# Kernel tuning notes

Hardware: AMD Instinct MI355X
Metric: run time of the kernel (lower is better)

The kernel has to match this reference:

```python
import jax, jax.numpy as jnp
import numpy as np

N_NODES = 50000
N_EDGES = 800000
D_IN = 96
D_HID = 256
D_OUT = 2
N_GRAPHS = 64


def _gin_conv(x, src, dst, W1, b1, W2, b2):
    # GINConv with eps=0: MLP(x + sum_{j in N(i)} x_j)
    agg = jax.ops.segment_sum(x[src], dst, num_segments=x.shape[0])
    h = x + agg
    h = jax.nn.relu(h @ W1 + b1)
    return h @ W2 + b2


def setup_inputs() -> dict:
    key = jax.random.key(0)
    ks = jax.random.split(key, 12)
    x = jax.random.normal(ks[0], (N_NODES, D_IN), dtype=jnp.float32)
    edge_index = jax.random.randint(ks[1], (2, N_EDGES), 0, N_NODES, dtype=jnp.int64)
    batch = jnp.sort(jax.random.randint(ks[2], (N_NODES,), 0, N_GRAPHS, dtype=jnp.int64))

    def lin(k, fan_in, shape):
        bound = 1.0 / np.sqrt(fan_in)
        return jax.random.uniform(k, shape, jnp.float32, -bound, bound)

    W1 = lin(ks[3], D_IN, (D_IN, D_HID)); b1 = lin(ks[4], D_IN, (D_HID,))
    W2 = lin(ks[5], D_HID, (D_HID, D_HID)); b2 = lin(ks[6], D_HID, (D_HID,))
    V1 = lin(ks[7], D_HID, (D_HID, D_HID)); c1 = lin(ks[8], D_HID, (D_HID,))
    V2 = lin(ks[9], D_HID, (D_HID, D_HID)); c2 = lin(ks[10], D_HID, (D_HID,))
    Wl = lin(ks[11], D_HID, (D_HID, D_OUT)); bl = jnp.zeros((D_OUT,), jnp.float32)
    return {"x": x, "edge_index": edge_index, "batch": batch,
            "W1": W1, "b1": b1, "W2": W2, "b2": b2,
            "V1": V1, "c1": c1, "V2": V2, "c2": c2,
            "Wl": Wl, "bl": bl}


def reference(x, edge_index, batch, W1, b1, W2, b2, V1, c1, V2, c2, Wl, bl):
    src, dst = edge_index[0], edge_index[1]
    h = jax.nn.relu(_gin_conv(x, src, dst, W1, b1, W2, b2))
    h = _gin_conv(h, src, dst, V1, c1, V2, c2)
    # global_mean_pool over batch ids
    sums = jax.ops.segment_sum(h, batch, num_segments=N_GRAPHS)
    counts = jax.ops.segment_sum(jnp.ones((h.shape[0], 1), h.dtype), batch,
                                 num_segments=N_GRAPHS)
    pooled = sums / jnp.maximum(counts, 1.0)
    # dropout p=0.1 is identity in eval mode
    return pooled @ Wl + bl
```

## Files before the change

### kernel.cpp

```cpp
#include <hip/hip_runtime.h>

#define N_NODES 50000
#define N_EDGES 800000
#define D_IN 96
#define D_HID 256
#define N_GRAPHS 64

#define SCAN_NB ((N_NODES + 255) / 256)

typedef __attribute__((ext_vector_type(8))) short bf16x8;
typedef __attribute__((ext_vector_type(4))) float f32x4;

__device__ __forceinline__ unsigned short f2bf(float f) {
    union { float f; unsigned int u; } v; v.f = f;
    unsigned int r = (v.u + 0x7FFFu + ((v.u >> 16) & 1u)) >> 16;
    return (unsigned short)r;
}
__device__ __forceinline__ float bfLo(unsigned int u) {
    union { unsigned int u; float f; } v; v.u = u << 16; return v.f;
}
__device__ __forceinline__ float bfHi(unsigned int u) {
    union { unsigned int u; float f; } v; v.u = u & 0xFFFF0000u; return v.f;
}
__device__ __forceinline__ unsigned int packbf(float a, float b) {
    return (unsigned int)f2bf(a) | ((unsigned int)f2bf(b) << 16);
}

__global__ void k_count(const int* __restrict__ dst, int* __restrict__ deg, int E) {
    int e = blockIdx.x * blockDim.x + threadIdx.x;
    if (e < E) atomicAdd(&deg[dst[e]], 1);
}

__global__ __launch_bounds__(256) void k_scan1(const int* __restrict__ deg,
                                               int* __restrict__ bsum, int n) {
    __shared__ int red[256];
    int tid = threadIdx.x;
    int i = blockIdx.x * 256 + tid;
    red[tid] = (i < n) ? deg[i] : 0;
    __syncthreads();
    for (int off = 128; off > 0; off >>= 1) {
        if (tid < off) red[tid] += red[tid + off];
        __syncthreads();
    }
    if (tid == 0) bsum[blockIdx.x] = red[0];
}

__global__ __launch_bounds__(256) void k_scan2(int* __restrict__ bsum, int nb) {
    __shared__ int s[256];
    int tid = threadIdx.x;
    int v = (tid < nb) ? bsum[tid] : 0;
    s[tid] = v;
    __syncthreads();
    for (int off = 1; off < 256; off <<= 1) {
        int t = (tid >= off) ? s[tid - off] : 0;
        __syncthreads();
        s[tid] += t;
        __syncthreads();
    }
    if (tid < nb) bsum[tid] = s[tid] - v;
}

__global__ __launch_bounds__(256) void k_scan3(const int* __restrict__ deg,
                                               const int* __restrict__ bsum,
                                               int* __restrict__ rp,
                                               int* __restrict__ wp, int n) {
    __shared__ int s[256];
    int tid = threadIdx.x;
    int i = blockIdx.x * 256 + tid;
    int v = (i < n) ? deg[i] : 0;
    s[tid] = v;
    __syncthreads();
    for (int off = 1; off < 256; off <<= 1) {
        int t = (tid >= off) ? s[tid - off] : 0;
        __syncthreads();
        s[tid] += t;
        __syncthreads();
    }
    if (i < n) {
        int excl = s[tid] - v + bsum[blockIdx.x];
        rp[i] = excl;
        wp[i] = excl;
    }
    if (blockIdx.x == 0 && tid == 0) rp[n] = N_EDGES;
}

__global__ void k_scatter(const int* __restrict__ src, const int* __restrict__ dst,
                          int* __restrict__ wp, int* __restrict__ csr, int E) {
    int e = blockIdx.x * blockDim.x + threadIdx.x;
    if (e < E) {
        int p = atomicAdd(&wp[dst[e]], 1);
        csr[p] = src[e];
    }
}

__global__ __launch_bounds__(256) void k_x2bf(const float* __restrict__ x,
                                              unsigned short* __restrict__ xb, int n4) {
    int i = blockIdx.x * 256 + threadIdx.x;
    if (i >= n4) return;
    float4 v = ((const float4*)x)[i];
    ((uint2*)xb)[i] = make_uint2(packbf(v.x, v.y), packbf(v.z, v.w));
}

#define ACCUM(acc, v)                                    \
    do {                                                 \
        acc[0] += bfLo((v).x); acc[1] += bfHi((v).x);    \
        acc[2] += bfLo((v).y); acc[3] += bfHi((v).y);    \
        acc[4] += bfLo((v).z); acc[5] += bfHi((v).z);    \
        acc[6] += bfLo((v).w); acc[7] += bfHi((v).w);    \
    } while (0)

__global__ __launch_bounds__(256) void k_agg96b(const unsigned short* __restrict__ xb,
                                                const int* __restrict__ rp,
                                                const int* __restrict__ csr,
                                                unsigned short* __restrict__ h0, int n) {
    int wid = blockIdx.x * 4 + (threadIdx.x >> 6);
    if (wid >= n) return;
    int lane = threadIdx.x & 63;
    int grp = lane / 12;
    int sub = lane % 12;
    int s = rp[wid], e = rp[wid + 1];
    const uint4* xp = (const uint4*)xb;
    float a[8] = {0.f, 0.f, 0.f, 0.f, 0.f, 0.f, 0.f, 0.f};
    float b[8] = {0.f, 0.f, 0.f, 0.f, 0.f, 0.f, 0.f, 0.f};
    if (lane < 48) {
        int j = s + grp;
        for (; j + 4 < e; j += 8) {
            int sc0 = csr[j];
            int sc1 = csr[j + 4];
            uint4 v0 = xp[(size_t)sc0 * 12 + sub];
            uint4 v1 = xp[(size_t)sc1 * 12 + sub];
            ACCUM(a, v0);
            ACCUM(b, v1);
        }
        if (j < e) {
            int sc0 = csr[j];
            uint4 v0 = xp[(size_t)sc0 * 12 + sub];
            ACCUM(a, v0);
        }
    }
#pragma unroll
    for (int i = 0; i < 8; i++) a[i] += b[i];
#pragma unroll
    for (int i = 0; i < 8; i++) a[i] += __shfl(a[i], lane + 24, 64);
#pragma unroll
    for (int i = 0; i < 8; i++) a[i] += __shfl(a[i], lane + 12, 64);
    if (lane < 12) {
        uint4 v = xp[(size_t)wid * 12 + sub];
        ACCUM(a, v);
        uint4 o;
        o.x = packbf(a[0], a[1]); o.y = packbf(a[2], a[3]);
        o.z = packbf(a[4], a[5]); o.w = packbf(a[6], a[7]);
        ((uint4*)h0)[(size_t)wid * 12 + sub] = o;
    }
}

__global__ __launch_bounds__(256) void k_agg256b(const unsigned short* __restrict__ h,
                                                 const int* __restrict__ rp,
                                                 const int* __restrict__ csr,
                                                 unsigned short* __restrict__ outb, int n) {
    int wid = blockIdx.x * 4 + (threadIdx.x >> 6);
    if (wid >= n) return;
    int lane = threadIdx.x & 63;
    int half = lane >> 5;
    int sub = lane & 31;
    int s = rp[wid], e = rp[wid + 1];
    const uint4* hp = (const uint4*)h;
    float a[8] = {0.f, 0.f, 0.f, 0.f, 0.f, 0.f, 0.f, 0.f};
    float b[8] = {0.f, 0.f, 0.f, 0.f, 0.f, 0.f, 0.f, 0.f};
    int j = s + half;
    for (; j + 2 < e; j += 4) {
        int sc0 = csr[j];
        int sc1 = csr[j + 2];
        uint4 v0 = hp[(size_t)sc0 * 32 + sub];
        uint4 v1 = hp[(size_t)sc1 * 32 + sub];
        ACCUM(a, v0);
        ACCUM(b, v1);
    }
    if (j < e) {
        int sc0 = csr[j];
        uint4 v0 = hp[(size_t)sc0 * 32 + sub];
        ACCUM(a, v0);
    }
#pragma unroll
    for (int i = 0; i < 8; i++) a[i] += b[i];
#pragma unroll
    for (int i = 0; i < 8; i++) a[i] += __shfl(a[i], sub + 32, 64);
    if (half == 0) {
        uint4 v = hp[(size_t)wid * 32 + sub];
        ACCUM(a, v);
        uint4 o;
        o.x = packbf(a[0], a[1]); o.y = packbf(a[2], a[3]);
        o.z = packbf(a[4], a[5]); o.w = packbf(a[6], a[7]);
        ((uint4*)outb)[(size_t)wid * 32 + sub] = o;
    }
}

__global__ __launch_bounds__(256) void k_wt(const float* __restrict__ W,
                                            unsigned short* __restrict__ Wt, int K) {
    int idx = blockIdx.x * 256 + threadIdx.x;
    if (idx >= K * 256) return;
    int k = idx >> 8;
    int n = idx & 255;
    Wt[(size_t)n * K + k] = f2bf(W[idx]);
}

template <int K1, bool RELU2>
__global__ __launch_bounds__(256) void fused_mlp(const unsigned short* __restrict__ A,
                                                 const unsigned short* __restrict__ W1t,
                                                 const float* __restrict__ bias1,
                                                 const unsigned short* __restrict__ W2t,
                                                 const float* __restrict__ bias2,
                                                 unsigned short* __restrict__ C, int M) {
    __shared__ unsigned short As[64][72];
    __shared__ unsigned short Bs[256][72];
    __shared__ unsigned short T1[64][264];
    const int tid = threadIdx.x;
    const int lane = tid & 63;
    const int wid = tid >> 6;
    const int wm = wid >> 1;
    const int wn = wid & 1;
    const int row0 = blockIdx.x * 64;

    f32x4 acc[2][8];
#pragma unroll
    for (int f = 0; f < 2; f++)
#pragma unroll
        for (int g = 0; g < 8; g++) acc[f][g] = (f32x4){0.f, 0.f, 0.f, 0.f};

    for (int kt = 0; kt < K1; kt += 64) {
        __syncthreads();
        {
            int m = tid >> 2;
            int kc = (tid & 3) * 16;
            int gr = row0 + m;
            uint4 w0 = make_uint4(0u, 0u, 0u, 0u), w1 = w0;
            int k = kt + kc;
            if (gr < M && k < K1) {
                w0 = *(const uint4*)&A[(size_t)gr * K1 + k];
                if (k + 8 < K1) w1 = *(const uint4*)&A[(size_t)gr * K1 + k + 8];
            }
            uint4* dst = (uint4*)&As[m][kc];
            dst[0] = w0; dst[1] = w1;
        }
#pragma unroll
        for (int p = 0; p < 2; p++) {
            int n = (tid >> 1) + p * 128;
            int kc = (tid & 1) * 32;
            uint4 w[4];
#pragma unroll
            for (int i = 0; i < 4; i++) {
                int k = kt + kc + i * 8;
                w[i] = (k < K1) ? *(const uint4*)&W1t[(size_t)n * K1 + k]
                                : make_uint4(0u, 0u, 0u, 0u);
            }
            uint4* dst = (uint4*)&Bs[n][kc];
#pragma unroll
            for (int i = 0; i < 4; i++) dst[i] = w[i];
        }
        __syncthreads();
#pragma unroll
        for (int ks = 0; ks < 2; ks++) {
            int ko = ks * 32 + (lane >> 4) * 8;
            bf16x8 af[2], bfr[8];
#pragma unroll
            for (int f = 0; f < 2; f++)
                af[f] = *(const bf16x8*)&As[wm * 32 + f * 16 + (lane & 15)][ko];
#pragma unroll
            for (int g = 0; g < 8; g++)
                bfr[g] = *(const bf16x8*)&Bs[wn * 128 + g * 16 + (lane & 15)][ko];
#pragma unroll
            for (int f = 0; f < 2; f++)
#pragma unroll
                for (int g = 0; g < 8; g++)
                    acc[f][g] = __builtin_amdgcn_mfma_f32_16x16x32_bf16(
                        af[f], bfr[g], acc[f][g], 0, 0, 0);
        }
    }

#pragma unroll
    for (int g = 0; g < 8; g++) {
        int col = wn * 128 + g * 16 + (lane & 15);
        float bb = bias1[col];
#pragma unroll
        for (int f = 0; f < 2; f++) {
#pragma unroll
            for (int r = 0; r < 4; r++) {
                int row = wm * 32 + f * 16 + (lane >> 4) * 4 + r;
                float v = fmaxf(acc[f][g][r] + bb, 0.f);
                T1[row][col] = f2bf(v);
            }
        }
    }
#pragma unroll
    for (int f = 0; f < 2; f++)
#pragma unroll
        for (int g = 0; g < 8; g++) acc[f][g] = (f32x4){0.f, 0.f, 0.f, 0.f};

    for (int kt = 0; kt < 256; kt += 64) {
        __syncthreads();
#pragma unroll
        for (int p = 0; p < 2; p++) {
            int n = (tid >> 1) + p * 128;
            int kc = (tid & 1) * 32;
            uint4 w[4];
#pragma unroll
            for (int i = 0; i < 4; i++) {
                int k = kt + kc + i * 8;
                w[i] = *(const uint4*)&W2t[(size_t)n * 256 + k];
            }
            uint4* dst = (uint4*)&Bs[n][kc];
#pragma unroll
            for (int i = 0; i < 4; i++) dst[i] = w[i];
        }
        __syncthreads();
#pragma unroll
        for (int ks = 0; ks < 2; ks++) {
            int ko = ks * 32 + (lane >> 4) * 8;
            bf16x8 af[2], bfr[8];
#pragma unroll
            for (int f = 0; f < 2; f++)
                af[f] = *(const bf16x8*)&T1[wm * 32 + f * 16 + (lane & 15)][kt + ko];
#pragma unroll
            for (int g = 0; g < 8; g++)
                bfr[g] = *(const bf16x8*)&Bs[wn * 128 + g * 16 + (lane & 15)][ko];
#pragma unroll
            for (int f = 0; f < 2; f++)
#pragma unroll
                for (int g = 0; g < 8; g++)
                    acc[f][g] = __builtin_amdgcn_mfma_f32_16x16x32_bf16(
                        af[f], bfr[g], acc[f][g], 0, 0, 0);
        }
    }

#pragma unroll
    for (int g = 0; g < 8; g++) {
        int n = wn * 128 + g * 16 + (lane & 15);
        float bb = bias2[n];
#pragma unroll
        for (int f = 0; f < 2; f++) {
#pragma unroll
            for (int r = 0; r < 4; r++) {
                int m = row0 + wm * 32 + f * 16 + (lane >> 4) * 4 + r;
                if (m < M) {
                    float v = acc[f][g][r] + bb;
                    if (RELU2) v = fmaxf(v, 0.f);
                    C[(size_t)m * 256 + n] = f2bf(v);
                }
            }
        }
    }
}

#define POOL_ROWS 64
__global__ __launch_bounds__(256) void k_pool_partial(const unsigned short* __restrict__ h,
                                                      const int* __restrict__ batch,
                                                      float* __restrict__ psum, int n) {
    int r0 = blockIdx.x * POOL_ROWS;
    int r1 = r0 + POOL_ROWS;
    if (r1 > n) r1 = n;
    if (r0 >= r1) return;
    int c = threadIdx.x;
    float acc = 0.f;
    int g = batch[r0];
    for (int r = r0; r < r1; r++) {
        int gr = batch[r];
        if (gr != g) {
            atomicAdd(&psum[g * 256 + c], acc);
            acc = 0.f;
            g = gr;
        }
        acc += bfLo((unsigned int)h[(size_t)r * 256 + c]);
    }
    atomicAdd(&psum[g * 256 + c], acc);
}

__device__ __forceinline__ int lower_bound_i(const int* __restrict__ a, int n, int v) {
    int lo = 0, hi = n;
    while (lo < hi) {
        int mid = (lo + hi) >> 1;
        if (a[mid] < v) lo = mid + 1; else hi = mid;
    }
    return lo;
}

__global__ __launch_bounds__(128) void k_head(const float* __restrict__ psum,
                                              const int* __restrict__ batch,
                                              const float* __restrict__ Wl,
                                              const float* __restrict__ bl,
                                              float* __restrict__ out, int n) {
    int tid = threadIdx.x;
    int g = tid >> 1, o = tid & 1;
    int s = lower_bound_i(batch, n, g);
    int e = lower_bound_i(batch, n, g + 1);
    float inv = 1.0f / (float)((e - s) > 1 ? (e - s) : 1);
    float sum = bl[o];
    for (int k = 0; k < 256; k++)
        sum = fmaf(psum[g * 256 + k] * inv, Wl[k * 2 + o], sum);
    out[g * 2 + o] = sum;
}

extern "C" void kernel_launch(void* const* d_in, const int* in_sizes, int n_in,
                              void* d_out, int out_size, void* d_ws, size_t ws_size,
                              hipStream_t stream) {
    const float* x = (const float*)d_in[0];
    const int* ei = (const int*)d_in[1];
    const int* batch = (const int*)d_in[2];
    const float* W1 = (const float*)d_in[3];
    const float* b1 = (const float*)d_in[4];
    const float* W2 = (const float*)d_in[5];
    const float* b2 = (const float*)d_in[6];
    const float* V1 = (const float*)d_in[7];
    const float* c1 = (const float*)d_in[8];
    const float* V2 = (const float*)d_in[9];
    const float* c2 = (const float*)d_in[10];
    const float* Wl = (const float*)d_in[11];
    const float* bl = (const float*)d_in[12];
    float* out = (float*)d_out;

    const int* srcp = ei;
    const int* dstp = ei + N_EDGES;

    char* ws = (char*)d_ws;
    size_t off = 0;
    auto alloc = [&](size_t bytes) {
        size_t o = off;
        off = (off + bytes + 255) & ~(size_t)255;
        return o;
    };
    size_t o_deg = alloc(sizeof(int) * (N_NODES + 1));
    size_t o_rp = alloc(sizeof(int) * (N_NODES + 1));
    size_t o_wp = alloc(sizeof(int) * (N_NODES + 1));
    size_t o_bsum = alloc(sizeof(int) * SCAN_NB);
    size_t o_csr = alloc(sizeof(int) * N_EDGES);
    size_t o_B1 = alloc(sizeof(unsigned short) * (size_t)N_NODES * D_HID);
    size_t o_B2 = alloc(sizeof(unsigned short) * (size_t)N_NODES * D_HID);
    size_t o_pool = alloc(sizeof(float) * N_GRAPHS * D_HID);
    size_t o_wt1 = alloc(sizeof(unsigned short) * D_IN * D_HID);
    size_t o_wt2 = alloc(sizeof(unsigned short) * D_HID * D_HID);
    size_t o_wv1 = alloc(sizeof(unsigned short) * D_HID * D_HID);
    size_t o_wv2 = alloc(sizeof(unsigned short) * D_HID * D_HID);
    (void)ws_size;

    int* deg = (int*)(ws + o_deg);
    int* rp = (int*)(ws + o_rp);
    int* wp = (int*)(ws + o_wp);
    int* bsum = (int*)(ws + o_bsum);
    int* csr = (int*)(ws + o_csr);
    unsigned short* B1 = (unsigned short*)(ws + o_B1);
    unsigned short* B2 = (unsigned short*)(ws + o_B2);
    float* psum = (float*)(ws + o_pool);
    unsigned short* wt1 = (unsigned short*)(ws + o_wt1);
    unsigned short* wt2 = (unsigned short*)(ws + o_wt2);
    unsigned short* wv1 = (unsigned short*)(ws + o_wv1);
    unsigned short* wv2 = (unsigned short*)(ws + o_wv2);

    hipMemsetAsync(deg, 0, sizeof(int) * (N_NODES + 1), stream);
    hipMemsetAsync(psum, 0, sizeof(float) * N_GRAPHS * D_HID, stream);

    k_wt<<<D_IN, 256, 0, stream>>>(W1, wt1, D_IN);
    k_wt<<<D_HID, 256, 0, stream>>>(W2, wt2, D_HID);
    k_wt<<<D_HID, 256, 0, stream>>>(V1, wv1, D_HID);
    k_wt<<<D_HID, 256, 0, stream>>>(V2, wv2, D_HID);

    k_count<<<(N_EDGES + 255) / 256, 256, 0, stream>>>(dstp, deg, N_EDGES);
    k_scan1<<<SCAN_NB, 256, 0, stream>>>(deg, bsum, N_NODES);
    k_scan2<<<1, 256, 0, stream>>>(bsum, SCAN_NB);
    k_scan3<<<SCAN_NB, 256, 0, stream>>>(deg, bsum, rp, wp, N_NODES);
    k_scatter<<<(N_EDGES + 255) / 256, 256, 0, stream>>>(srcp, dstp, wp, csr, N_EDGES);

    k_x2bf<<<(N_NODES * D_IN / 4 + 255) / 256, 256, 0, stream>>>(x, B1, N_NODES * D_IN / 4);

    int mlpgrid = (N_NODES + 63) / 64;

    k_agg96b<<<(N_NODES + 3) / 4, 256, 0, stream>>>(B1, rp, csr, B2, N_NODES);
    fused_mlp<96, true><<<mlpgrid, 256, 0, stream>>>(B2, wt1, b1, wt2, b2, B1, N_NODES);

    k_agg256b<<<(N_NODES + 3) / 4, 256, 0, stream>>>(B1, rp, csr, B2, N_NODES);
    fused_mlp<256, false><<<mlpgrid, 256, 0, stream>>>(B2, wv1, c1, wv2, c2, B1, N_NODES);

    k_pool_partial<<<(N_NODES + POOL_ROWS - 1) / POOL_ROWS, 256, 0, stream>>>(
        B1, batch, psum, N_NODES);
    k_head<<<1, 128, 0, stream>>>(psum, batch, Wl, bl, out, N_NODES);
}
```

Baseline: 333.1 us.

## Load MFMA operands directly from global memory, drop LDS staging and syncs

The fused MLP kernel no longer stages A and weight tiles through shared memory. Each wave now loads its MFMA fragments straight from global memory, relying on L1/L2 caching of the small weight matrices, which removes most __syncthreads and the LDS round trip. The intermediate hidden tile keeps LDS but uses an XOR swizzle instead of padding, which shrinks the shared footprint and can raise occupancy. The trade-off is redundant global and cache traffic, since the two waves sharing a row tile (and the two sharing a column tile) each fetch the same operands. Global load latency is also exposed directly to the MFMA loop.

```diff
diff --git a/kernel.cpp b/kernel.cpp
--- a/kernel.cpp
+++ b/kernel.cpp
@@ -211,136 +211,95 @@
                                                  const unsigned short* __restrict__ W2t,
                                                  const float* __restrict__ bias2,
                                                  unsigned short* __restrict__ C, int M) {
-    __shared__ unsigned short As[64][72];
-    __shared__ unsigned short Bs[256][72];
-    __shared__ unsigned short T1[64][264];
+    __shared__ unsigned short T1[64 * 256];
     const int tid = threadIdx.x;
     const int lane = tid & 63;
     const int wid = tid >> 6;
     const int wm = wid >> 1;
     const int wn = wid & 1;
     const int row0 = blockIdx.x * 64;
-
+    const int l15 = lane & 15;
+    const int l4 = lane >> 4;
+
+    const bf16x8 ZV = {0, 0, 0, 0, 0, 0, 0, 0};
     f32x4 acc[2][8];
 #pragma unroll
     for (int f = 0; f < 2; f++)
 #pragma unroll
         for (int g = 0; g < 8; g++) acc[f][g] = (f32x4){0.f, 0.f, 0.f, 0.f};
 
-    for (int kt = 0; kt < K1; kt += 64) {
-        __syncthreads();
-        {
-            int m = tid >> 2;
-            int kc = (tid & 3) * 16;
-            int gr = row0 + m;
-            uint4 w0 = make_uint4(0u, 0u, 0u, 0u), w1 = w0;
-            int k = kt + kc;
-            if (gr < M && k < K1) {
-                w0 = *(const uint4*)&A[(size_t)gr * K1 + k];
-                if (k + 8 < K1) w1 = *(const uint4*)&A[(size_t)gr * K1 + k + 8];
+    const int r0 = row0 + wm * 32 + l15;
+    const int n0 = wn * 128 + l15;
+#pragma unroll 2
+    for (int ks = 0; ks < K1 / 32; ks++) {
+        int k = ks * 32 + l4 * 8;
+        bf16x8 af[2], bfr[8];
+#pragma unroll
+        for (int f = 0; f < 2; f++) {
+            int r = r0 + f * 16;
+            af[f] = (r < M) ? *(const bf16x8*)&A[(size_t)r * K1 + k] : ZV;
+        }
+#pragma unroll
+        for (int g = 0; g < 8; g++)
+            bfr[g] = *(const bf16x8*)&W1t[(size_t)(n0 + g * 16) * K1 + k];
+#pragma unroll
+        for (int f = 0; f < 2; f++)
+#pragma unroll
+            for (int g = 0; g < 8; g++)
+                acc[f][g] = __builtin_amdgcn_mfma_f32_16x16x32_bf16(
+                    af[f], bfr[g], acc[f][g], 0, 0, 0);
+    }
+
+#pragma unroll
+    for (int g = 0; g < 8; g++) {
+        int col = wn * 128 + g * 16 + l15;
+        float bb = bias1[col];
+#pragma unroll
+        for (int f = 0; f < 2; f++) {
+#pragma unroll
+            for (int r = 0; r < 4; r++) {
+                int row = wm * 32 + f * 16 + l4 * 4 + r;
+                float v = fmaxf(acc[f][g][r] + bb, 0.f);
+                int sw = (((col >> 3) ^ (row & 7)) << 3) | (col & 7);
+                T1[row * 256 + sw] = f2bf(v);
             }
-            uint4* dst = (uint4*)&As[m][kc];
-            dst[0] = w0; dst[1] = w1;
-        }
-#pragma unroll
-        for (int p = 0; p < 2; p++) {
-            int n = (tid >> 1) + p * 128;
-            int kc = (tid & 1) * 32;
-            uint4 w[4];
-#pragma unroll
-            for (int i = 0; i < 4; i++) {
-                int k = kt + kc + i * 8;
-                w[i] = (k < K1) ? *(const uint4*)&W1t[(size_t)n * K1 + k]
-                                : make_uint4(0u, 0u, 0u, 0u);
-            }
-            uint4* dst = (uint4*)&Bs[n][kc];
-#pragma unroll
-            for (int i = 0; i < 4; i++) dst[i] = w[i];
-        }
-        __syncthreads();
-#pragma unroll
-        for (int ks = 0; ks < 2; ks++) {
-            int ko = ks * 32 + (lane >> 4) * 8;
-            bf16x8 af[2], bfr[8];
-#pragma unroll
-            for (int f = 0; f < 2; f++)
-                af[f] = *(const bf16x8*)&As[wm * 32 + f * 16 + (lane & 15)][ko];
+        }
+    }
+#pragma unroll
+    for (int f = 0; f < 2; f++)
+#pragma unroll
+        for (int g = 0; g < 8; g++) acc[f][g] = (f32x4){0.f, 0.f, 0.f, 0.f};
+    __syncthreads();
+
+#pragma unroll 2
+    for (int ks = 0; ks < 8; ks++) {
+        int k = ks * 32 + l4 * 8;
+        bf16x8 af[2], bfr[8];
+#pragma unroll
+        for (int f = 0; f < 2; f++) {
+            int row = wm * 32 + f * 16 + l15;
+            af[f] = *(const bf16x8*)&T1[row * 256 + (((k >> 3) ^ (row & 7)) << 3)];
+        }
+#pragma unroll
+        for (int g = 0; g < 8; g++)
+            bfr[g] = *(const bf16x8*)&W2t[(size_t)(n0 + g * 16) * 256 + k];
+#pragma unroll
+        for (int f = 0; f < 2; f++)
 #pragma unroll
             for (int g = 0; g < 8; g++)
-                bfr[g] = *(const bf16x8*)&Bs[wn * 128 + g * 16 + (lane & 15)][ko];
-#pragma unroll
-            for (int f = 0; f < 2; f++)
-#pragma unroll
-                for (int g = 0; g < 8; g++)
-                    acc[f][g] = __builtin_amdgcn_mfma_f32_16x16x32_bf16(
-                        af[f], bfr[g], acc[f][g], 0, 0, 0);
-        }
+                acc[f][g] = __builtin_amdgcn_mfma_f32_16x16x32_bf16(
+                    af[f], bfr[g], acc[f][g], 0, 0, 0);
     }
 
 #pragma unroll
     for (int g = 0; g < 8; g++) {
-        int col = wn * 128 + g * 16 + (lane & 15);
-        float bb = bias1[col];
+        int n = wn * 128 + g * 16 + l15;
+        float bb = bias2[n];
 #pragma unroll
         for (int f = 0; f < 2; f++) {
 #pragma unroll
             for (int r = 0; r < 4; r++) {
-                int row = wm * 32 + f * 16 + (lane >> 4) * 4 + r;
-                float v = fmaxf(acc[f][g][r] + bb, 0.f);
-                T1[row][col] = f2bf(v);
-            }
-        }
-    }
-#pragma unroll
-    for (int f = 0; f < 2; f++)
-#pragma unroll
-        for (int g = 0; g < 8; g++) acc[f][g] = (f32x4){0.f, 0.f, 0.f, 0.f};
-
-    for (int kt = 0; kt < 256; kt += 64) {
-        __syncthreads();
-#pragma unroll
-        for (int p = 0; p < 2; p++) {
-            int n = (tid >> 1) + p * 128;
-            int kc = (tid & 1) * 32;
-            uint4 w[4];
-#pragma unroll
-            for (int i = 0; i < 4; i++) {
-                int k = kt + kc + i * 8;
-                w[i] = *(const uint4*)&W2t[(size_t)n * 256 + k];
-            }
-            uint4* dst = (uint4*)&Bs[n][kc];
-#pragma unroll
-            for (int i = 0; i < 4; i++) dst[i] = w[i];
-        }
-        __syncthreads();
-#pragma unroll
-        for (int ks = 0; ks < 2; ks++) {
-            int ko = ks * 32 + (lane >> 4) * 8;
-            bf16x8 af[2], bfr[8];
-#pragma unroll
-            for (int f = 0; f < 2; f++)
-                af[f] = *(const bf16x8*)&T1[wm * 32 + f * 16 + (lane & 15)][kt + ko];
-#pragma unroll
-            for (int g = 0; g < 8; g++)
-                bfr[g] = *(const bf16x8*)&Bs[wn * 128 + g * 16 + (lane & 15)][ko];
-#pragma unroll
-            for (int f = 0; f < 2; f++)
-#pragma unroll
-                for (int g = 0; g < 8; g++)
-                    acc[f][g] = __builtin_amdgcn_mfma_f32_16x16x32_bf16(
-                        af[f], bfr[g], acc[f][g], 0, 0, 0);
-        }
-    }
-
-#pragma unroll
-    for (int g = 0; g < 8; g++) {
-        int n = wn * 128 + g * 16 + (lane & 15);
-        float bb = bias2[n];
-#pragma unroll
-        for (int f = 0; f < 2; f++) {
-#pragma unroll
-            for (int r = 0; r < 4; r++) {
-                int m = row0 + wm * 32 + f * 16 + (lane >> 4) * 4 + r;
+                int m = row0 + wm * 32 + f * 16 + l4 * 4 + r;
                 if (m < M) {
                     float v = acc[f][g][r] + bb;
                     if (RELU2) v = fmaxf(v, 0.f);
```

Result: slower. 390.7 us (+17.3%).
